# Kernel tuning notes

Measured on AMD Instinct MI355X. Metric: run time of the kernel, lower is better.

Reference implementation:

```python
import jax, jax.numpy as jnp
import numpy as np

L, D, H, FF = 4, 256, 8, 4 * 256  # num_layers, d_model, nhead, ffn hidden
DK = D // H
EPS = 1e-5


def _ln(x, g, b):
    mu = jnp.mean(x, axis=-1, keepdims=True)
    var = jnp.mean(jnp.square(x - mu), axis=-1, keepdims=True)
    return (x - mu) * jax.lax.rsqrt(var + EPS) * g + b


def setup_inputs() -> dict:
    key = jax.random.key(0)
    ks = jax.random.split(key, 16)
    B, N = 8, 1024
    s = 0.02
    return {
        "x": jax.random.normal(ks[0], (B, N, D), jnp.float32),
        "coords": jax.random.normal(ks[1], (B, N, 3), jnp.float32),
        "Wq": jax.random.normal(ks[2], (L, D, D), jnp.float32) * s,
        "bq": jnp.zeros((L, D), jnp.float32),
        "Wk": jax.random.normal(ks[3], (L, D, D), jnp.float32) * s,
        "bk": jnp.zeros((L, D), jnp.float32),
        "Wv": jax.random.normal(ks[4], (L, D, D), jnp.float32) * s,
        "bv": jnp.zeros((L, D), jnp.float32),
        "alpha": jnp.full((L,), 0.1, jnp.float32),
        "W1": jax.random.normal(ks[5], (L, D, FF), jnp.float32) * s,
        "b1": jnp.zeros((L, FF), jnp.float32),
        "W2": jax.random.normal(ks[6], (L, FF, D), jnp.float32) * s,
        "b2": jnp.zeros((L, D), jnp.float32),
        "g1": jnp.ones((L, D), jnp.float32),
        "be1": jnp.zeros((L, D), jnp.float32),
        "g2": jnp.ones((L, D), jnp.float32),
        "be2": jnp.zeros((L, D), jnp.float32),
    }


def reference(x, coords, Wq, bq, Wk, bk, Wv, bv, alpha, W1, b1, W2, b2, g1, be1, g2, be2):
    B, N, _ = x.shape
    # Per-batch pairwise coord dot products (same math as the BN x BN matmul
    # sliced per batch in the original, computed without the cross-batch waste).
    G0 = jnp.einsum("bnc,bmc->bnm", coords, coords)  # [B,N,N]
    scale = 1.0 / jnp.sqrt(jnp.float32(DK))
    for i in range(L):
        q = (x @ Wq[i] + bq[i]).reshape(B, N, H, DK)
        k = (x @ Wk[i] + bk[i]).reshape(B, N, H, DK)
        v = (x @ Wv[i] + bv[i]).reshape(B, N, H, DK)
        scores = jnp.einsum("bnhd,bmhd->bhnm", q, k) * scale + (alpha[i] * G0)[:, None]
        attn = jax.nn.softmax(scores, axis=-1)
        out = jnp.einsum("bhnm,bmhd->bnhd", attn, v).reshape(B, N, D)
        x = _ln(x + out, g1[i], be1[i])
        ff = jnp.maximum(x @ W1[i] + b1[i], 0.0) @ W2[i] + b2[i]
        x = _ln(x + ff, g2[i], be2[i])
    return x
```

## Files before the change

### kernel.cpp

```cpp
#include <hip/hip_runtime.h>
#include <hip/hip_bf16.h>

#define BB 8
#define NN 1024
#define DD 256
#define HH 8
#define DK 32
#define FFN 1024
#define NLAYERS 4
#define MM (BB * NN)
#define ROW_ELEMS (MM * DD)

#define QSCALE 0.2550655192922103f
#define LOG2E  1.4426950408889634f

typedef unsigned short ushort_t;
typedef __attribute__((ext_vector_type(8))) short bf16x8;
typedef __attribute__((ext_vector_type(4))) short bf16x4;
typedef __attribute__((ext_vector_type(4))) float f32x4;

__device__ __forceinline__ f32x4 mfma16(bf16x4 a, bf16x4 b, f32x4 c) {
#if __has_builtin(__builtin_amdgcn_mfma_f32_16x16x16bf16_1k)
    return __builtin_amdgcn_mfma_f32_16x16x16bf16_1k(a, b, c, 0, 0, 0);
#elif defined(__AMDGCN__)
    f32x4 d;
    asm volatile("v_mfma_f32_16x16x16_bf16 %0, %1, %2, %3"
                 : "=v"(d)
                 : "v"(a), "v"(b), "v"(c));
    return d;
#else
    return c;
#endif
}

__device__ __forceinline__ ushort_t f2b(float f) {
    __hip_bfloat16 h = __float2bfloat16(f);
    return *reinterpret_cast<ushort_t*>(&h);
}

__device__ __forceinline__ float fast_exp2(float x) {
#if __has_builtin(__builtin_amdgcn_exp2f)
    return __builtin_amdgcn_exp2f(x);
#else
    return exp2f(x);
#endif
}

__device__ __forceinline__ void async_ld16(const void* g, void* l) {
    __builtin_amdgcn_global_load_lds((const __attribute__((address_space(1))) void*)g,
                                     (__attribute__((address_space(3))) void*)l, 16, 0, 0);
}

__global__ __launch_bounds__(256) void copy_in_kernel(const float4* __restrict__ in,
                                                      float4* __restrict__ xf,
                                                      ushort4* __restrict__ xb, int n4) {
    int i = blockIdx.x * 256 + threadIdx.x;
    if (i < n4) {
        float4 v = in[i];
        xf[i] = v;
        ushort4 b = {f2b(v.x), f2b(v.y), f2b(v.z), f2b(v.w)};
        xb[i] = b;
    }
}

__global__ __launch_bounds__(256) void prep_kernel(const float* __restrict__ Wq,
                                                   const float* __restrict__ Wk,
                                                   const float* __restrict__ Wv,
                                                   const float* __restrict__ W1,
                                                   const float* __restrict__ W2,
                                                   const float* __restrict__ bq,
                                                   const float* __restrict__ bk,
                                                   const float* __restrict__ bv,
                                                   ushort_t* __restrict__ wqkvt,
                                                   ushort_t* __restrict__ w1t,
                                                   ushort_t* __restrict__ w2t,
                                                   float* __restrict__ bqkv) {
    const int id = blockIdx.x;
    const int layer = id / 707;
    const int r = id % 707;
    const int tid = threadIdx.x;

    if (r >= 704) {
        const int chunk = r - 704;
        const float* src = (chunk == 0) ? bq : (chunk == 1) ? bk : bv;
        bqkv[layer * 768 + chunk * 256 + tid] = src[layer * 256 + tid];
        return;
    }

    const float* src;
    ushort_t* dst;
    int R, C, x, y;
    if (r < 192) {
        const int w = r >> 6, rr = r & 63;
        src = ((w == 0) ? Wq : (w == 1) ? Wk : Wv) + (size_t)layer * 65536;
        dst = wqkvt + (size_t)layer * 196608 + w * 65536;
        R = 256; C = 256; x = rr & 7; y = rr >> 3;
    } else if (r < 448) {
        const int rr = r - 192;
        src = W1 + (size_t)layer * 262144;
        dst = w1t + (size_t)layer * 262144;
        R = 256; C = 1024; x = rr & 31; y = rr >> 5;
    } else {
        const int rr = r - 448;
        src = W2 + (size_t)layer * 262144;
        dst = w2t + (size_t)layer * 262144;
        R = 1024; C = 256; x = rr & 7; y = rr >> 3;
    }
    const int r0 = y * 32, c0 = x * 32;
    __shared__ float tile[32][33];
    const int tx = tid & 31, ty = tid >> 5;
#pragma unroll
    for (int i = 0; i < 4; ++i)
        tile[ty + 8 * i][tx] = src[(size_t)(r0 + ty + 8 * i) * C + (c0 + tx)];
    __syncthreads();
#pragma unroll
    for (int i = 0; i < 4; ++i)
        dst[(size_t)(c0 + ty + 8 * i) * R + (r0 + tx)] = f2b(tile[tx][ty + 8 * i]);
}

template <int MODE, int BM>
__global__ __launch_bounds__(256) void mfma_gemm_kernel(const ushort_t* __restrict__ A,
                                                        const ushort_t* __restrict__ Bt,
                                                        const float* __restrict__ bias,
                                                        void* __restrict__ C0,
                                                        void* __restrict__ C1,
                                                        void* __restrict__ C2,
                                                        const float* __restrict__ coords,
                                                        const float* __restrict__ alpha, int layer,
                                                        int K, int ldc) {
    constexpr int NI = BM / 32;
    __shared__ ushort_t As0[2][BM * 32];
    __shared__ ushort_t As1[2][BM * 32];
    __shared__ ushort_t Bs0[2][128 * 32];
    __shared__ ushort_t Bs1[2][128 * 32];

    const int t    = threadIdx.x;
    const int bm   = blockIdx.y * BM;
    const int bn   = blockIdx.x * 128;
    const int wave = t >> 6, lane = t & 63;
    const int wm   = (wave >> 1) * (BM / 2), wn = (wave & 1) * 64;
    const int quad = lane >> 4, l16 = lane & 15;

    const int srow = t >> 2;
    const int scol = (t & 3) * 8;

    f32x4 acc[NI][4];
#pragma unroll
    for (int i = 0; i < NI; ++i)
#pragma unroll
        for (int j = 0; j < 4; ++j) {
            f32x4 z = {0.f, 0.f, 0.f, 0.f};
            acc[i][j] = z;
        }

    auto stage = [&](int pb, int k0) {
        async_ld16(A + (size_t)(bm + srow) * K + k0 + scol, As0[pb] + wave * 512);
        if constexpr (BM == 128)
            async_ld16(A + (size_t)(bm + 64 + srow) * K + k0 + scol, As0[pb] + 2048 + wave * 512);
        async_ld16(Bt + (size_t)(bn + srow) * K + k0 + scol, Bs0[pb] + wave * 512);
        async_ld16(Bt + (size_t)(bn + 64 + srow) * K + k0 + scol, Bs0[pb] + 2048 + wave * 512);
        async_ld16(A + (size_t)(bm + srow) * K + k0 + 32 + scol, As1[pb] + wave * 512);
        if constexpr (BM == 128)
            async_ld16(A + (size_t)(bm + 64 + srow) * K + k0 + 32 + scol, As1[pb] + 2048 + wave * 512);
        async_ld16(Bt + (size_t)(bn + srow) * K + k0 + 32 + scol, Bs1[pb] + wave * 512);
        async_ld16(Bt + (size_t)(bn + 64 + srow) * K + k0 + 32 + scol, Bs1[pb] + 2048 + wave * 512);
    };

    stage(0, 0);
    int pb = 0;
    for (int k0 = 0; k0 < K; k0 += 64, pb ^= 1) {
        __syncthreads();

        if (k0 + 64 < K) stage(pb ^ 1, k0 + 64);

        bf16x8 af0[NI], af1[NI], bf0[4], bf1[4];
#pragma unroll
        for (int i = 0; i < NI; ++i) {
            af0[i] = *(const bf16x8*)(As0[pb] + (wm + i * 16 + l16) * 32 + quad * 8);
            af1[i] = *(const bf16x8*)(As1[pb] + (wm + i * 16 + l16) * 32 + quad * 8);
        }
#pragma unroll
        for (int j = 0; j < 4; ++j) {
            bf0[j] = *(const bf16x8*)(Bs0[pb] + (wn + j * 16 + l16) * 32 + quad * 8);
            bf1[j] = *(const bf16x8*)(Bs1[pb] + (wn + j * 16 + l16) * 32 + quad * 8);
        }
#pragma unroll
        for (int i = 0; i < NI; ++i)
#pragma unroll
            for (int j = 0; j < 4; ++j) {
                acc[i][j] = __builtin_amdgcn_mfma_f32_16x16x32_bf16(af0[i], bf0[j], acc[i][j], 0, 0, 0);
                acc[i][j] = __builtin_amdgcn_mfma_f32_16x16x32_bf16(af1[i], bf1[j], acc[i][j], 0, 0, 0);
            }
    }

    const float av = (MODE == 2) ? alpha[layer] : 0.f;

#pragma unroll
    for (int j = 0; j < 4; ++j) {
        const int col = bn + wn + j * 16 + l16;
        const float bsv = bias[col];
#pragma unroll
        for (int i = 0; i < NI; ++i) {
            const int row0 = bm + wm + i * 16 + quad * 4;
            if (MODE == 2) {
                const int bb2 = row0 >> 10, nn0 = row0 & 1023;
                const int which = col >> 8, rem = col & 255;
                const int h = rem >> 5, d = rem & 31;
                const size_t bh = (size_t)((bb2 << 3) + h);
                if (which == 2) {
                    ushort4 pk;
                    pk.x = f2b(acc[i][j][0] + bsv);
                    pk.y = f2b(acc[i][j][1] + bsv);
                    pk.z = f2b(acc[i][j][2] + bsv);
                    pk.w = f2b(acc[i][j][3] + bsv);
                    *(ushort4*)&((ushort_t*)C2)[(bh * DK + d) * NN + nn0] = pk;
                } else {
#pragma unroll
                    for (int r = 0; r < 4; ++r) {
                        const float v = acc[i][j][r] + bsv;
                        const int nn = nn0 + r;
                        if (which == 0) {
                            ((ushort_t*)C0)[(bh * NN + nn) * 64 + d] = f2b(v * QSCALE);
                            ushort_t ext = 0;
                            if (d < 3) ext = f2b(av * LOG2E * coords[(size_t)(bb2 * NN + nn) * 3 + d]);
                            ((ushort_t*)C0)[(bh * NN + nn) * 64 + 32 + d] = ext;
                        } else {
                            ((ushort_t*)C1)[(bh * NN + nn) * 64 + d] = f2b(v);
                            ushort_t ext = 0;
                            if (d < 3) ext = f2b(coords[(size_t)(bb2 * NN + nn) * 3 + d]);
                            ((ushort_t*)C1)[(bh * NN + nn) * 64 + 32 + d] = ext;
                        }
                    }
                }
            } else {
#pragma unroll
                for (int r = 0; r < 4; ++r) {
                    float v = acc[i][j][r] + bsv;
                    if (MODE == 0)
                        ((float*)C0)[(size_t)(row0 + r) * ldc + col] = v;
                    else
                        ((ushort_t*)C0)[(size_t)(row0 + r) * ldc + col] = f2b(fmaxf(v, 0.f));
                }
            }
        }
    }
}

__global__ __launch_bounds__(512) void ff2ln_kernel(const ushort_t* __restrict__ A,
                                                    const ushort_t* __restrict__ Bt,
                                                    const float* __restrict__ bias,
                                                    const float* __restrict__ xres,
                                                    const float* __restrict__ g,
                                                    const float* __restrict__ be,
                                                    float* __restrict__ xout,
                                                    ushort_t* __restrict__ xb) {
    constexpr int K = FFN;
    __shared__ ushort_t As0[2][32 * 32];
    __shared__ ushort_t As1[2][32 * 32];
    __shared__ ushort_t Bs0[2][256 * 32];
    __shared__ ushort_t Bs1[2][256 * 32];
    __shared__ float redS[8][32];
    __shared__ float redQ[8][32];

    const int t = threadIdx.x;
    const int bm = blockIdx.x * 32;
    const int wave = t >> 6, lane = t & 63;
    const int quad = lane >> 4, l16 = lane & 15;
    const int wn = wave * 32;
    const int srow = t >> 2;
    const int scol = (t & 3) * 8;

    f32x4 acc[2][2];
#pragma unroll
    for (int i = 0; i < 2; ++i)
#pragma unroll
        for (int j = 0; j < 2; ++j) {
            f32x4 z = {0.f, 0.f, 0.f, 0.f};
            acc[i][j] = z;
        }

    auto stage = [&](int pb, int k0) {
        if (t < 128) {
            async_ld16(A + (size_t)(bm + srow) * K + k0 + scol, As0[pb] + wave * 512);
        } else if (t < 256) {
            async_ld16(A + (size_t)(bm + srow - 32) * K + k0 + 32 + scol, As1[pb] + (wave - 2) * 512);
        }
        async_ld16(Bt + (size_t)srow * K + k0 + scol, Bs0[pb] + wave * 512);
        async_ld16(Bt + (size_t)(128 + srow) * K + k0 + scol, Bs0[pb] + 4096 + wave * 512);
        async_ld16(Bt + (size_t)srow * K + k0 + 32 + scol, Bs1[pb] + wave * 512);
        async_ld16(Bt + (size_t)(128 + srow) * K + k0 + 32 + scol, Bs1[pb] + 4096 + wave * 512);
    };

    stage(0, 0);
    int pb = 0;
    for (int k0 = 0; k0 < K; k0 += 64, pb ^= 1) {
        __syncthreads();

        if (k0 + 64 < K) stage(pb ^ 1, k0 + 64);

        bf16x8 af0[2], af1[2], bf0[2], bf1[2];
#pragma unroll
        for (int i = 0; i < 2; ++i) {
            af0[i] = *(const bf16x8*)(As0[pb] + (i * 16 + l16) * 32 + quad * 8);
            af1[i] = *(const bf16x8*)(As1[pb] + (i * 16 + l16) * 32 + quad * 8);
        }
#pragma unroll
        for (int j = 0; j < 2; ++j) {
            bf0[j] = *(const bf16x8*)(Bs0[pb] + (wn + j * 16 + l16) * 32 + quad * 8);
            bf1[j] = *(const bf16x8*)(Bs1[pb] + (wn + j * 16 + l16) * 32 + quad * 8);
        }
#pragma unroll
        for (int i = 0; i < 2; ++i)
#pragma unroll
            for (int j = 0; j < 2; ++j) {
                acc[i][j] = __builtin_amdgcn_mfma_f32_16x16x32_bf16(af0[i], bf0[j], acc[i][j], 0, 0, 0);
                acc[i][j] = __builtin_amdgcn_mfma_f32_16x16x32_bf16(af1[i], bf1[j], acc[i][j], 0, 0, 0);
            }
    }

    float mean[2][4], rstd[2][4];

    {
        float sum_[2][4];
#pragma unroll
        for (int i = 0; i < 2; ++i)
#pragma unroll
            for (int r = 0; r < 4; ++r) sum_[i][r] = 0.f;
#pragma unroll
        for (int j = 0; j < 2; ++j) {
            const int col = wn + j * 16 + l16;
            const float bj = bias[col];
#pragma unroll
            for (int i = 0; i < 2; ++i) {
                const int row = bm + i * 16 + quad * 4;
#pragma unroll
                for (int r = 0; r < 4; ++r) {
                    const float v = acc[i][j][r] + bj + xres[(size_t)(row + r) * DD + col];
                    acc[i][j][r] = v;
                    sum_[i][r] += v;
                }
            }
        }
#pragma unroll
        for (int i = 0; i < 2; ++i)
#pragma unroll
            for (int r = 0; r < 4; ++r) {
                float s = sum_[i][r];
                s += __shfl_xor(s, 1);
                s += __shfl_xor(s, 2);
                s += __shfl_xor(s, 4);
                s += __shfl_xor(s, 8);
                sum_[i][r] = s;
            }
        if (l16 == 0) {
#pragma unroll
            for (int i = 0; i < 2; ++i)
#pragma unroll
                for (int r = 0; r < 4; ++r) redS[wave][i * 16 + quad * 4 + r] = sum_[i][r];
        }
        __syncthreads();
#pragma unroll
        for (int i = 0; i < 2; ++i)
#pragma unroll
            for (int r = 0; r < 4; ++r) {
                const int rl = i * 16 + quad * 4 + r;
                float s = 0.f;
#pragma unroll
                for (int w = 0; w < 8; ++w) s += redS[w][rl];
                mean[i][r] = s * (1.0f / 256.0f);
            }
    }

    {
        float sq_[2][4];
#pragma unroll
        for (int i = 0; i < 2; ++i)
#pragma unroll
            for (int r = 0; r < 4; ++r) sq_[i][r] = 0.f;
#pragma unroll
        for (int j = 0; j < 2; ++j)
#pragma unroll
            for (int i = 0; i < 2; ++i)
#pragma unroll
                for (int r = 0; r < 4; ++r) {
                    const float d = acc[i][j][r] - mean[i][r];
                    sq_[i][r] += d * d;
                }
#pragma unroll
        for (int i = 0; i < 2; ++i)
#pragma unroll
            for (int r = 0; r < 4; ++r) {
                float s = sq_[i][r];
                s += __shfl_xor(s, 1);
                s += __shfl_xor(s, 2);
                s += __shfl_xor(s, 4);
                s += __shfl_xor(s, 8);
                sq_[i][r] = s;
            }
        if (l16 == 0) {
#pragma unroll
            for (int i = 0; i < 2; ++i)
#pragma unroll
                for (int r = 0; r < 4; ++r) redQ[wave][i * 16 + quad * 4 + r] = sq_[i][r];
        }
        __syncthreads();
#pragma unroll
        for (int i = 0; i < 2; ++i)
#pragma unroll
            for (int r = 0; r < 4; ++r) {
                const int rl = i * 16 + quad * 4 + r;
                float s = 0.f;
#pragma unroll
                for (int w = 0; w < 8; ++w) s += redQ[w][rl];
                rstd[i][r] = rsqrtf(s * (1.0f / 256.0f) + 1e-5f);
            }
    }

#pragma unroll
    for (int j = 0; j < 2; ++j) {
        const int col = wn + j * 16 + l16;
        const float gv = g[col];
        const float bev = be[col];
#pragma unroll
        for (int i = 0; i < 2; ++i) {
            const int row = bm + i * 16 + quad * 4;
#pragma unroll
            for (int r = 0; r < 4; ++r) {
                const float y = (acc[i][j][r] - mean[i][r]) * rstd[i][r] * gv + bev;
                xout[(size_t)(row + r) * DD + col] = y;
                xb[(size_t)(row + r) * DD + col] = f2b(y);
            }
        }
    }
}

__global__ __launch_bounds__(256, 2) void attn8_kernel(const ushort_t* __restrict__ Qa,
                                                       const ushort_t* __restrict__ Ka,
                                                       const ushort_t* __restrict__ Vt,
                                                       float* __restrict__ aout) {
    const int b = blockIdx.x, h = blockIdx.y, n0 = blockIdx.z * 64;
    const int t = threadIdx.x, wave = t >> 6, lane = t & 63;
    const int quad = lane >> 4, l16 = lane & 15;
    const int bh = b * HH + h;

    __shared__ __align__(16) char smem[56320];
    ushort_t (*Ks)[64][72] = (ushort_t (*)[64][72])smem;
    ushort_t (*Vs)[32][72] = (ushort_t (*)[32][72])(smem + 36864);
    float    (*Om)[64][36] = (float (*)[64][36])smem;
    float    (*Lm)[64]     = (float (*)[64])(smem + 55296);

    bf16x8 aq[4][2];
#pragma unroll
    for (int s = 0; s < 4; ++s) {
        const ushort_t* qp = Qa + ((size_t)bh * NN + n0 + s * 16 + l16) * 64 + quad * 8;
        aq[s][0] = *(const bf16x8*)qp;
        aq[s][1] = *(const bf16x8*)(qp + 32);
    }

    const f32x4 z = {0.f, 0.f, 0.f, 0.f};
    f32x4 acc[4][2];
    float lsum[4];
#pragma unroll
    for (int s = 0; s < 4; ++s) { acc[s][0] = z; acc[s][1] = z; lsum[s] = 0.f; }

    const ushort_t* kg = Ka + ((size_t)bh * NN + wave * 256) * 64;
    const ushort_t* vg = Vt + (size_t)bh * DK * NN + wave * 256;

    const int srow = lane >> 3, sch = (lane & 7) * 8;

    uint4 kreg[8], vreg[4];
#pragma unroll
    for (int i = 0; i < 8; ++i) kreg[i] = *(const uint4*)(kg + (size_t)(i * 8 + srow) * 64 + sch);
#pragma unroll
    for (int i = 0; i < 4; ++i) vreg[i] = *(const uint4*)(vg + (size_t)(i * 8 + srow) * NN + sch);

    for (int kt = 0; kt < 4; ++kt) {
#pragma unroll
        for (int i = 0; i < 8; ++i) *(uint4*)&Ks[wave][i * 8 + srow][sch] = kreg[i];
#pragma unroll
        for (int i = 0; i < 4; ++i) *(uint4*)&Vs[wave][i * 8 + srow][sch] = vreg[i];

        bf16x8 bk0[4], bk1[4];
#pragma unroll
        for (int jt = 0; jt < 4; ++jt) {
            bk0[jt] = *(const bf16x8*)&Ks[wave][jt * 16 + l16][quad * 8];
            bk1[jt] = *(const bf16x8*)&Ks[wave][jt * 16 + l16][32 + quad * 8];
        }
        bf16x4 vfrag[2][4];
#pragma unroll
        for (int g = 0; g < 2; ++g)
#pragma unroll
            for (int jt = 0; jt < 4; ++jt)
                vfrag[g][jt] = *(const bf16x4*)&Vs[wave][g * 16 + l16][jt * 16 + quad * 4];

        if (kt < 3) {
            const ushort_t* kg2 = kg + (size_t)(kt + 1) * 64 * 64;
            const ushort_t* vg2 = vg + (kt + 1) * 64;
#pragma unroll
            for (int i = 0; i < 8; ++i)
                kreg[i] = *(const uint4*)(kg2 + (size_t)(i * 8 + srow) * 64 + sch);
#pragma unroll
            for (int i = 0; i < 4; ++i)
                vreg[i] = *(const uint4*)(vg2 + (size_t)(i * 8 + srow) * NN + sch);
        }

#pragma unroll
        for (int s = 0; s < 4; ++s) {
            f32x4 st[4];
            __builtin_amdgcn_s_setprio(1);
#pragma unroll
            for (int jt = 0; jt < 4; ++jt) {
                st[jt] = __builtin_amdgcn_mfma_f32_16x16x32_bf16(bk0[jt], aq[s][0], z, 0, 0, 0);
                st[jt] = __builtin_amdgcn_mfma_f32_16x16x32_bf16(bk1[jt], aq[s][1], st[jt], 0, 0, 0);
            }
            __builtin_amdgcn_s_setprio(0);
            bf16x4 pf[4];
            float ls = 0.f;
#pragma unroll
            for (int jt = 0; jt < 4; ++jt) {
                float e0 = fast_exp2(st[jt][0]);
                float e1 = fast_exp2(st[jt][1]);
                float e2 = fast_exp2(st[jt][2]);
                float e3 = fast_exp2(st[jt][3]);
                ls += (e0 + e1) + (e2 + e3);
                pf[jt][0] = (short)f2b(e0);
                pf[jt][1] = (short)f2b(e1);
                pf[jt][2] = (short)f2b(e2);
                pf[jt][3] = (short)f2b(e3);
            }
            lsum[s] += ls;
            __builtin_amdgcn_s_setprio(1);
#pragma unroll
            for (int jt = 0; jt < 4; ++jt) {
                acc[s][0] = mfma16(vfrag[0][jt], pf[jt], acc[s][0]);
                acc[s][1] = mfma16(vfrag[1][jt], pf[jt], acc[s][1]);
            }
            __builtin_amdgcn_s_setprio(0);
        }
    }

#pragma unroll
    for (int s = 0; s < 4; ++s) {
        lsum[s] += __shfl_xor(lsum[s], 16);
        lsum[s] += __shfl_xor(lsum[s], 32);
    }

    __syncthreads();
    if (quad == 0) {
#pragma unroll
        for (int s = 0; s < 4; ++s) Lm[wave][s * 16 + l16] = lsum[s];
    }

#pragma unroll
    for (int s = 0; s < 4; ++s) {
        const int q = s * 16 + l16;
#pragma unroll
        for (int g = 0; g < 2; ++g) {
            float4 v = {acc[s][g][0], acc[s][g][1], acc[s][g][2], acc[s][g][3]};
            *(float4*)&Om[wave][q][g * 16 + quad * 4] = v;
        }
    }
    __syncthreads();

    {
        const int q = t >> 2, dseg = (t & 3) * 8;
        const float inv = 1.0f / (Lm[0][q] + Lm[1][q] + Lm[2][q] + Lm[3][q]);
        float* op = aout + (size_t)(b * NN + n0 + q) * DD + h * DK + dseg;
        float4 s0 = {0.f, 0.f, 0.f, 0.f}, s1 = {0.f, 0.f, 0.f, 0.f};
#pragma unroll
        for (int w = 0; w < 4; ++w) {
            float4 a = *(const float4*)&Om[w][q][dseg];
            float4 c = *(const float4*)&Om[w][q][dseg + 4];
            s0.x += a.x; s0.y += a.y; s0.z += a.z; s0.w += a.w;
            s1.x += c.x; s1.y += c.y; s1.z += c.z; s1.w += c.w;
        }
        float4 o0 = {s0.x * inv, s0.y * inv, s0.z * inv, s0.w * inv};
        float4 o1 = {s1.x * inv, s1.y * inv, s1.z * inv, s1.w * inv};
        *(float4*)op = o0;
        *(float4*)(op + 4) = o1;
    }
}

__global__ __launch_bounds__(256) void addln_kernel(const float* __restrict__ x,
                                                    ushort_t* __restrict__ xb,
                                                    const float* __restrict__ delta, int dstride,
                                                    const float* __restrict__ g,
                                                    const float* __restrict__ be,
                                                    float* __restrict__ xout) {
    const int row  = blockIdx.x * 4 + (threadIdx.x >> 6);
    const int lane = threadIdx.x & 63;
    const size_t base = (size_t)row * DD + lane * 4;

    float4 xv = *(const float4*)(x + base);
    float4 dl = *(const float4*)(delta + (size_t)row * dstride + lane * 4);
    float v0 = xv.x + dl.x, v1 = xv.y + dl.y, v2 = xv.z + dl.z, v3 = xv.w + dl.w;

    float s = v0 + v1 + v2 + v3;
#pragma unroll
    for (int off = 32; off; off >>= 1) s += __shfl_xor(s, off);
    const float mean = s * (1.0f / 256.0f);

    float d0 = v0 - mean, d1 = v1 - mean, d2 = v2 - mean, d3 = v3 - mean;
    float s2 = d0 * d0 + d1 * d1 + d2 * d2 + d3 * d3;
#pragma unroll
    for (int off = 32; off; off >>= 1) s2 += __shfl_xor(s2, off);
    const float rs = rsqrtf(s2 * (1.0f / 256.0f) + 1e-5f);

    float4 gv = *(const float4*)(g + lane * 4);
    float4 bv = *(const float4*)(be + lane * 4);
    float y0 = d0 * rs * gv.x + bv.x;
    float y1 = d1 * rs * gv.y + bv.y;
    float y2 = d2 * rs * gv.z + bv.z;
    float y3 = d3 * rs * gv.w + bv.w;

    float4 o = {y0, y1, y2, y3};
    *(float4*)(xout + base) = o;
    ushort4 ob = {f2b(y0), f2b(y1), f2b(y2), f2b(y3)};
    *(ushort4*)(xb + base) = ob;
}

extern "C" void kernel_launch(void* const* d_in, const int* in_sizes, int n_in,
                              void* d_out, int out_size, void* d_ws, size_t ws_size,
                              hipStream_t stream) {
    const float* x      = (const float*)d_in[0];
    const float* coords = (const float*)d_in[1];
    const float* Wq     = (const float*)d_in[2];
    const float* bq     = (const float*)d_in[3];
    const float* Wk     = (const float*)d_in[4];
    const float* bk     = (const float*)d_in[5];
    const float* Wv     = (const float*)d_in[6];
    const float* bv     = (const float*)d_in[7];
    const float* alpha  = (const float*)d_in[8];
    const float* W1     = (const float*)d_in[9];
    const float* b1     = (const float*)d_in[10];
    const float* W2     = (const float*)d_in[11];
    const float* b2     = (const float*)d_in[12];
    const float* g1     = (const float*)d_in[13];
    const float* be1    = (const float*)d_in[14];
    const float* g2     = (const float*)d_in[15];
    const float* be2    = (const float*)d_in[16];

    float* ws = (float*)d_ws;
    float*    xf    = ws;
    ushort_t* xb    = (ushort_t*)(ws + 2097152);
    ushort_t* Qa    = (ushort_t*)(ws + 3145728);
    ushort_t* Ka    = (ushort_t*)(ws + 5242880);
    ushort_t* Vt    = (ushort_t*)(ws + 7340032);
    float*    aout  = ws + 8388608;
    ushort_t* wqkvt = (ushort_t*)(ws + 10485760);
    ushort_t* w1t   = (ushort_t*)(ws + 10878976);
    ushort_t* w2t   = (ushort_t*)(ws + 11403264);
    float*    bqkv  = ws + 11927552;

    ushort_t* hidden = Qa;

    prep_kernel<<<NLAYERS * 707, 256, 0, stream>>>(Wq, Wk, Wv, W1, W2, bq, bk, bv,
                                                   wqkvt, w1t, w2t, bqkv);

    copy_in_kernel<<<ROW_ELEMS / 4 / 256, 256, 0, stream>>>((const float4*)x, (float4*)xf,
                                                            (ushort4*)xb, ROW_ELEMS / 4);

    for (int i = 0; i < NLAYERS; ++i) {
        mfma_gemm_kernel<2, 64><<<dim3(6, 128), 256, 0, stream>>>(
            xb, wqkvt + (size_t)i * 196608, bqkv + i * 768, Qa, Ka, Vt,
            coords, alpha, i, 256, 0);

        attn8_kernel<<<dim3(8, 8, 16), 256, 0, stream>>>(Qa, Ka, Vt, aout);

        addln_kernel<<<MM / 4, 256, 0, stream>>>(xf, xb, aout, 256, g1 + i * 256, be1 + i * 256, xf);

        mfma_gemm_kernel<1, 128><<<dim3(8, 64), 256, 0, stream>>>(
            xb, w1t + (size_t)i * 262144, b1 + i * 1024, hidden, nullptr, nullptr,
            nullptr, nullptr, 0, 256, 1024);

        ff2ln_kernel<<<MM / 32, 512, 0, stream>>>(
            hidden, w2t + (size_t)i * 262144, b2 + i * 256, xf,
            g2 + i * 256, be2 + i * 256,
            (i == NLAYERS - 1) ? (float*)d_out : xf, xb);
    }
}
```

Baseline: 410.3 us.

## Fuse FFN up-projection into FFN-down+LayerNorm kernel, keep hidden in LDS

Replaces the separate W1 GEMM and the W2+LayerNorm kernel with one kernel per 32-row block. It computes the ReLU hidden activations in four 256-column chunks into shared memory and then runs the W2 GEMM from shared memory. This removes the global round trip of the 8192x1024 bf16 hidden tensor and one launch per layer. In exchange, W1 and W2 weights are re-streamed for every 32-row block, LDS use grows (about 96KB), and occupancy may drop. Separately, the constant coordinate and zero padding in the Q/K extension columns are written once up front instead of by the QKV GEMM epilogue every layer.

```diff
diff --git a/kernel.cpp b/kernel.cpp
--- a/kernel.cpp
+++ b/kernel.cpp
@@ -60,6 +60,29 @@
         xf[i] = v;
         ushort4 b = {f2b(v.x), f2b(v.y), f2b(v.z), f2b(v.w)};
         xb[i] = b;
+    }
+}
+
+__global__ __launch_bounds__(256) void qkext_init_kernel(const float* __restrict__ coords,
+                                                         ushort_t* __restrict__ Qa,
+                                                         ushort_t* __restrict__ Ka) {
+    const int id = blockIdx.x * 256 + threadIdx.x;
+    const int bh = id >> 10, n = id & 1023;
+    const int b = bh >> 3;
+    ushort_t buf[32];
+#pragma unroll
+    for (int d = 0; d < 32; ++d) buf[d] = 0;
+    buf[0] = f2b(coords[(size_t)(b * NN + n) * 3 + 0]);
+    buf[1] = f2b(coords[(size_t)(b * NN + n) * 3 + 1]);
+    buf[2] = f2b(coords[(size_t)(b * NN + n) * 3 + 2]);
+    ushort_t* kp = Ka + ((size_t)bh * NN + n) * 64 + 32;
+    ushort_t* qp = Qa + ((size_t)bh * NN + n) * 64 + 32;
+    const uint4* b4 = (const uint4*)buf;
+    uint4 z4 = {0u, 0u, 0u, 0u};
+#pragma unroll
+    for (int c = 0; c < 4; ++c) {
+        *(uint4*)(kp + c * 8) = b4[c];
+        *(uint4*)(qp + c * 8) = z4;
     }
 }
 
@@ -221,14 +244,11 @@
                         const int nn = nn0 + r;
                         if (which == 0) {
                             ((ushort_t*)C0)[(bh * NN + nn) * 64 + d] = f2b(v * QSCALE);
-                            ushort_t ext = 0;
-                            if (d < 3) ext = f2b(av * LOG2E * coords[(size_t)(bb2 * NN + nn) * 3 + d]);
-                            ((ushort_t*)C0)[(bh * NN + nn) * 64 + 32 + d] = ext;
+                            if (d < 3)
+                                ((ushort_t*)C0)[(bh * NN + nn) * 64 + 32 + d] =
+                                    f2b(av * LOG2E * coords[(size_t)(bb2 * NN + nn) * 3 + d]);
                         } else {
                             ((ushort_t*)C1)[(bh * NN + nn) * 64 + d] = f2b(v);
-                            ushort_t ext = 0;
-                            if (d < 3) ext = f2b(coords[(size_t)(bb2 * NN + nn) * 3 + d]);
-                            ((ushort_t*)C1)[(bh * NN + nn) * 64 + 32 + d] = ext;
                         }
                     }
                 }
@@ -246,17 +266,18 @@
     }
 }
 
-__global__ __launch_bounds__(512) void ff2ln_kernel(const ushort_t* __restrict__ A,
-                                                    const ushort_t* __restrict__ Bt,
-                                                    const float* __restrict__ bias,
-                                                    const float* __restrict__ xres,
-                                                    const float* __restrict__ g,
-                                                    const float* __restrict__ be,
-                                                    float* __restrict__ xout,
-                                                    ushort_t* __restrict__ xb) {
-    constexpr int K = FFN;
-    __shared__ ushort_t As0[2][32 * 32];
-    __shared__ ushort_t As1[2][32 * 32];
+__global__ __launch_bounds__(512) void ffn_ln_kernel(const ushort_t* __restrict__ A,
+                                                     const ushort_t* __restrict__ W1t,
+                                                     const ushort_t* __restrict__ W2t,
+                                                     const float* __restrict__ b1,
+                                                     const float* __restrict__ b2,
+                                                     const float* __restrict__ xres,
+                                                     const float* __restrict__ g,
+                                                     const float* __restrict__ be,
+                                                     float* __restrict__ xout,
+                                                     ushort_t* __restrict__ xb) {
+    __shared__ ushort_t Ha[32][32][32];
+    __shared__ ushort_t Asf[8][32][32];
     __shared__ ushort_t Bs0[2][256 * 32];
     __shared__ ushort_t Bs1[2][256 * 32];
     __shared__ float redS[8][32];
@@ -267,42 +288,60 @@
     const int wave = t >> 6, lane = t & 63;
     const int quad = lane >> 4, l16 = lane & 15;
     const int wn = wave * 32;
-    const int srow = t >> 2;
     const int scol = (t & 3) * 8;
 
-    f32x4 acc[2][2];
+#pragma unroll
+    for (int c = 0; c < 2; ++c) {
+        const int arow = (t >> 2) & 31;
+        const int acol = (c * 4 + (t >> 7)) * 32 + scol;
+        async_ld16(A + (size_t)(bm + arow) * 256 + acol,
+                   (ushort_t*)Asf + c * 4096 + wave * 512);
+    }
+
+    auto stageB1 = [&](int pb, int step) {
+        const int nbase = (step >> 2) * 256;
+        const int k0 = (step & 3) * 64;
+#pragma unroll
+        for (int c = 0; c < 2; ++c) {
+            const int brow = nbase + c * 128 + (t >> 2);
+            async_ld16(W1t + (size_t)brow * 256 + k0 + scol, Bs0[pb] + c * 4096 + wave * 512);
+            async_ld16(W1t + (size_t)brow * 256 + k0 + 32 + scol, Bs1[pb] + c * 4096 + wave * 512);
+        }
+    };
+    auto stageB2 = [&](int pb, int step) {
+        const int k0 = step * 64;
+#pragma unroll
+        for (int c = 0; c < 2; ++c) {
+            const int brow = c * 128 + (t >> 2);
+            async_ld16(W2t + (size_t)brow * 1024 + k0 + scol, Bs0[pb] + c * 4096 + wave * 512);
+            async_ld16(W2t + (size_t)brow * 1024 + k0 + 32 + scol, Bs1[pb] + c * 4096 + wave * 512);
+        }
+    };
+
+    f32x4 acc1[2][2], acc2[2][2];
 #pragma unroll
     for (int i = 0; i < 2; ++i)
 #pragma unroll
         for (int j = 0; j < 2; ++j) {
             f32x4 z = {0.f, 0.f, 0.f, 0.f};
-            acc[i][j] = z;
-        }
-
-    auto stage = [&](int pb, int k0) {
-        if (t < 128) {
-            async_ld16(A + (size_t)(bm + srow) * K + k0 + scol, As0[pb] + wave * 512);
-        } else if (t < 256) {
-            async_ld16(A + (size_t)(bm + srow - 32) * K + k0 + 32 + scol, As1[pb] + (wave - 2) * 512);
-        }
-        async_ld16(Bt + (size_t)srow * K + k0 + scol, Bs0[pb] + wave * 512);
-        async_ld16(Bt + (size_t)(128 + srow) * K + k0 + scol, Bs0[pb] + 4096 + wave * 512);
-        async_ld16(Bt + (size_t)srow * K + k0 + 32 + scol, Bs1[pb] + wave * 512);
-        async_ld16(Bt + (size_t)(128 + srow) * K + k0 + 32 + scol, Bs1[pb] + 4096 + wave * 512);
-    };
-
-    stage(0, 0);
+            acc1[i][j] = z;
+            acc2[i][j] = z;
+        }
+
+    stageB1(0, 0);
     int pb = 0;
-    for (int k0 = 0; k0 < K; k0 += 64, pb ^= 1) {
+
+    for (int step = 0; step < 16; ++step, pb ^= 1) {
         __syncthreads();
-
-        if (k0 + 64 < K) stage(pb ^ 1, k0 + 64);
-
+        if (step < 15) stageB1(pb ^ 1, step + 1);
+        else stageB2(pb ^ 1, 0);
+
+        const int ks = step & 3;
         bf16x8 af0[2], af1[2], bf0[2], bf1[2];
 #pragma unroll
         for (int i = 0; i < 2; ++i) {
-            af0[i] = *(const bf16x8*)(As0[pb] + (i * 16 + l16) * 32 + quad * 8);
-            af1[i] = *(const bf16x8*)(As1[pb] + (i * 16 + l16) * 32 + quad * 8);
+            af0[i] = *(const bf16x8*)&Asf[2 * ks][i * 16 + l16][quad * 8];
+            af1[i] = *(const bf16x8*)&Asf[2 * ks + 1][i * 16 + l16][quad * 8];
         }
 #pragma unroll
         for (int j = 0; j < 2; ++j) {
@@ -313,8 +352,56 @@
         for (int i = 0; i < 2; ++i)
 #pragma unroll
             for (int j = 0; j < 2; ++j) {
-                acc[i][j] = __builtin_amdgcn_mfma_f32_16x16x32_bf16(af0[i], bf0[j], acc[i][j], 0, 0, 0);
-                acc[i][j] = __builtin_amdgcn_mfma_f32_16x16x32_bf16(af1[i], bf1[j], acc[i][j], 0, 0, 0);
+                acc1[i][j] = __builtin_amdgcn_mfma_f32_16x16x32_bf16(af0[i], bf0[j], acc1[i][j], 0, 0, 0);
+                acc1[i][j] = __builtin_amdgcn_mfma_f32_16x16x32_bf16(af1[i], bf1[j], acc1[i][j], 0, 0, 0);
+            }
+
+        if (ks == 3) {
+            const int nc = step >> 2;
+#pragma unroll
+            for (int j = 0; j < 2; ++j) {
+                const int col = nc * 256 + wn + j * 16 + l16;
+                const float bj = b1[col];
+#pragma unroll
+                for (int i = 0; i < 2; ++i)
+#pragma unroll
+                    for (int r = 0; r < 4; ++r) {
+                        const int row = i * 16 + quad * 4 + r;
+                        Ha[nc * 8 + wave][row][j * 16 + l16] =
+                            f2b(fmaxf(acc1[i][j][r] + bj, 0.f));
+                    }
+            }
+#pragma unroll
+            for (int i = 0; i < 2; ++i)
+#pragma unroll
+                for (int j = 0; j < 2; ++j) {
+                    f32x4 z = {0.f, 0.f, 0.f, 0.f};
+                    acc1[i][j] = z;
+                }
+        }
+    }
+
+    for (int step = 0; step < 16; ++step, pb ^= 1) {
+        __syncthreads();
+        if (step < 15) stageB2(pb ^ 1, step + 1);
+
+        bf16x8 af0[2], af1[2], bf0[2], bf1[2];
+#pragma unroll
+        for (int i = 0; i < 2; ++i) {
+            af0[i] = *(const bf16x8*)&Ha[2 * step][i * 16 + l16][quad * 8];
+            af1[i] = *(const bf16x8*)&Ha[2 * step + 1][i * 16 + l16][quad * 8];
+        }
+#pragma unroll
+        for (int j = 0; j < 2; ++j) {
+            bf0[j] = *(const bf16x8*)(Bs0[pb] + (wn + j * 16 + l16) * 32 + quad * 8);
+            bf1[j] = *(const bf16x8*)(Bs1[pb] + (wn + j * 16 + l16) * 32 + quad * 8);
+        }
+#pragma unroll
+        for (int i = 0; i < 2; ++i)
+#pragma unroll
+            for (int j = 0; j < 2; ++j) {
+                acc2[i][j] = __builtin_amdgcn_mfma_f32_16x16x32_bf16(af0[i], bf0[j], acc2[i][j], 0, 0, 0);
+                acc2[i][j] = __builtin_amdgcn_mfma_f32_16x16x32_bf16(af1[i], bf1[j], acc2[i][j], 0, 0, 0);
             }
     }
 
@@ -329,14 +416,14 @@
 #pragma unroll
         for (int j = 0; j < 2; ++j) {
             const int col = wn + j * 16 + l16;
-            const float bj = bias[col];
+            const float bj = b2[col];
 #pragma unroll
             for (int i = 0; i < 2; ++i) {
                 const int row = bm + i * 16 + quad * 4;
 #pragma unroll
                 for (int r = 0; r < 4; ++r) {
-                    const float v = acc[i][j][r] + bj + xres[(size_t)(row + r) * DD + col];
-                    acc[i][j][r] = v;
+                    const float v = acc2[i][j][r] + bj + xres[(size_t)(row + r) * DD + col];
+                    acc2[i][j][r] = v;
                     sum_[i][r] += v;
                 }
             }
@@ -383,7 +470,7 @@
             for (int i = 0; i < 2; ++i)
 #pragma unroll
                 for (int r = 0; r < 4; ++r) {
-                    const float d = acc[i][j][r] - mean[i][r];
+                    const float d = acc2[i][j][r] - mean[i][r];
                     sq_[i][r] += d * d;
                 }
 #pragma unroll
@@ -426,7 +513,7 @@
             const int row = bm + i * 16 + quad * 4;
 #pragma unroll
             for (int r = 0; r < 4; ++r) {
-                const float y = (acc[i][j][r] - mean[i][r]) * rstd[i][r] * gv + bev;
+                const float y = (acc2[i][j][r] - mean[i][r]) * rstd[i][r] * gv + bev;
                 xout[(size_t)(row + r) * DD + col] = y;
                 xb[(size_t)(row + r) * DD + col] = f2b(y);
             }
@@ -652,13 +739,13 @@
     ushort_t* w2t   = (ushort_t*)(ws + 11403264);
     float*    bqkv  = ws + 11927552;
 
-    ushort_t* hidden = Qa;
-
     prep_kernel<<<NLAYERS * 707, 256, 0, stream>>>(Wq, Wk, Wv, W1, W2, bq, bk, bv,
                                                    wqkvt, w1t, w2t, bqkv);
 
     copy_in_kernel<<<ROW_ELEMS / 4 / 256, 256, 0, stream>>>((const float4*)x, (float4*)xf,
                                                             (ushort4*)xb, ROW_ELEMS / 4);
+
+    qkext_init_kernel<<<256, 256, 0, stream>>>(coords, Qa, Ka);
 
     for (int i = 0; i < NLAYERS; ++i) {
         mfma_gemm_kernel<2, 64><<<dim3(6, 128), 256, 0, stream>>>(
@@ -669,12 +756,9 @@
 
         addln_kernel<<<MM / 4, 256, 0, stream>>>(xf, xb, aout, 256, g1 + i * 256, be1 + i * 256, xf);
 
-        mfma_gemm_kernel<1, 128><<<dim3(8, 64), 256, 0, stream>>>(
-            xb, w1t + (size_t)i * 262144, b1 + i * 1024, hidden, nullptr, nullptr,
-            nullptr, nullptr, 0, 256, 1024);
-
-        ff2ln_kernel<<<MM / 32, 512, 0, stream>>>(
-            hidden, w2t + (size_t)i * 262144, b2 + i * 256, xf,
+        ffn_ln_kernel<<<MM / 32, 512, 0, stream>>>(
+            xb, w1t + (size_t)i * 262144, w2t + (size_t)i * 262144,
+            b1 + i * 1024, b2 + i * 256, xf,
             g2 + i * 256, be2 + i * 256,
             (i == NLAYERS - 1) ? (float*)d_out : xf, xb);
     }
```

Result: faster. 396.6 us (-3.3%).
